# Kernel tuning notes

Hardware: AMD Instinct MI355X
Metric: run time of the kernel (lower is better)

Reference implementation:

```python
import jax, jax.numpy as jnp
import numpy as np

B, T, H, NH = 4, 2048, 2048, 16
HD = H // NH
SCALE = HD ** -0.5

def setup_inputs() -> dict:
    key = jax.random.key(0)
    ks = jax.random.split(key, 9)
    s = H ** -0.5
    return {
        "x": jax.random.normal(ks[0], (B, T, H), jnp.float32),
        "q_w": jax.random.normal(ks[1], (H, H), jnp.float32) * s,
        "q_b": jnp.zeros((H,), jnp.float32),
        "k_w": jax.random.normal(ks[2], (H, H), jnp.float32) * s,
        "k_b": jnp.zeros((H,), jnp.float32),
        "v_w": jax.random.normal(ks[3], (H, H), jnp.float32) * s,
        "v_b": jnp.zeros((H,), jnp.float32),
        "o_w": jax.random.normal(ks[4], (H, H), jnp.float32) * s,
        "o_b": jnp.zeros((H,), jnp.float32),
    }

def reference(x, q_w, q_b, k_w, k_b, v_w, v_b, o_w, o_b):
    Bd, Td, Hd = x.shape
    # projections (torch Linear: y = x @ W^T + b)
    q = (x @ q_w.T + q_b).reshape(Bd, Td, NH, HD).transpose(0, 2, 1, 3)  # [B,nh,T,hd]
    k = (x @ k_w.T + k_b).reshape(Bd, Td, NH, HD).transpose(0, 2, 1, 3)
    v = (x @ v_w.T + v_b).reshape(Bd, Td, NH, HD).transpose(0, 2, 1, 3)
    scores = jnp.einsum('bhqd,bhkd->bhqk', q, k) * SCALE  # [B,nh,T,T]
    causal = jnp.tril(jnp.ones((Td, Td), dtype=bool))
    scores = jnp.where(causal, scores, -jnp.inf)
    probs = jax.nn.softmax(scores, axis=-1)
    ctx = jnp.einsum('bhqk,bhkd->bhqd', probs, v)  # [B,nh,T,hd]
    ctx = ctx.transpose(0, 2, 1, 3).reshape(Bd, Td, Hd)
    return ctx @ o_w.T + o_b
```

## Files before the change

### kernel.cpp

```cpp
#include <hip/hip_runtime.h>
#include <stdint.h>

#define B_SZ 4
#define T_SEQ 2048
#define H_DIM 2048
#define NH_ 16
#define HD_ 128
#define MTOK (B_SZ * T_SEQ)

typedef __attribute__((ext_vector_type(8))) short bf16x8;
typedef __attribute__((ext_vector_type(4))) float f32x4;
typedef __attribute__((ext_vector_type(4))) unsigned short u16x4;

__device__ __forceinline__ unsigned short f2b(float f) {
  union { float f; uint32_t u; } x; x.f = f;
  uint32_t r = x.u + 0x7FFFu + ((x.u >> 16) & 1u);
  return (unsigned short)(r >> 16);
}

__device__ __forceinline__ void gload16(const void* g, void* l) {
  __builtin_amdgcn_global_load_lds((const __attribute__((address_space(1))) void*)g,
                                   (__attribute__((address_space(3))) void*)l, 16, 0, 0);
}

__global__ void cvt_bf16_k(const float* __restrict__ in, unsigned short* __restrict__ out, int n4) {
  for (int i = blockIdx.x * blockDim.x + threadIdx.x; i < n4; i += gridDim.x * blockDim.x) {
    float4 v = ((const float4*)in)[i];
    u16x4 o;
    o[0] = f2b(v.x); o[1] = f2b(v.y); o[2] = f2b(v.z); o[3] = f2b(v.w);
    ((u16x4*)out)[i] = o;
  }
}

__global__ void cvt4_bf16_k(const float* __restrict__ s0, const float* __restrict__ s1,
                            const float* __restrict__ s2, const float* __restrict__ s3,
                            unsigned short* __restrict__ d0, unsigned short* __restrict__ d1,
                            unsigned short* __restrict__ d2, unsigned short* __restrict__ d3) {
  const int n4each = (H_DIM * H_DIM) / 4;
  for (int i = blockIdx.x * blockDim.x + threadIdx.x; i < 4 * n4each; i += gridDim.x * blockDim.x) {
    int sel = i >> 20, j = i & (n4each - 1);
    const float* src = sel == 0 ? s0 : sel == 1 ? s1 : sel == 2 ? s2 : s3;
    unsigned short* dst = sel == 0 ? d0 : sel == 1 ? d1 : sel == 2 ? d2 : d3;
    float4 v = ((const float4*)src)[j];
    u16x4 o;
    o[0] = f2b(v.x); o[1] = f2b(v.y); o[2] = f2b(v.z); o[3] = f2b(v.w);
    ((u16x4*)dst)[j] = o;
  }
}

template <int MODE>
__global__ __launch_bounds__(512, 2) void gemm256_k(const unsigned short* __restrict__ A,
                                                    const unsigned short* __restrict__ W,
                                                    const float* __restrict__ bias,
                                                    void* __restrict__ outp,
                                                    float oscale) {
  constexpr int K = H_DIM;
  constexpr int NT = K / 64;
  __shared__ __align__(16) unsigned short Al[2][256 * 64];
  __shared__ __align__(16) unsigned short Bl[2][256 * 64];

  const int tid = threadIdx.x;
  const int w = tid >> 6, l = tid & 63;
  const int g = l >> 4, ln = l & 15;
  const int wr = w >> 2, wc = w & 3;

  const int bid = blockIdx.x + gridDim.x * blockIdx.y;
  const int fid = ((bid & 7) << 5) | (bid >> 3);
  const int col0 = (fid & 7) * 256;
  const int row0 = (fid >> 3) * 256;

  const char* Ag = (const char*)A;
  const char* Wg = (const char*)W;

  const int srow = l >> 3;
  const int sbyte = ((l & 7) * 16) ^ (srow << 4);

#define ST_A(t2, b2, c)                                                                 \
  gload16(Ag + (((size_t)(row0 + (c) * 8 + srow)) * K + (t2) * 64) * 2 + sbyte,         \
          (char*)&Al[b2][0] + (c) * 1024)
#define ST_B(t2, b2, c)                                                                 \
  gload16(Wg + (((size_t)(col0 + (c) * 8 + srow)) * K + (t2) * 64) * 2 + sbyte,         \
          (char*)&Bl[b2][0] + (c) * 1024)
#define STAGE_A0(t2, b2) do { ST_A(t2, b2, w);  ST_A(t2, b2, 16 + w); } while (0)
#define STAGE_A1(t2, b2) do { ST_A(t2, b2, 8 + w); ST_A(t2, b2, 24 + w); } while (0)
#define STAGE_B0(t2, b2) do { int c_ = (w >> 2) * 8 + (w & 3); ST_B(t2, b2, c_); ST_B(t2, b2, 16 + c_); } while (0)
#define STAGE_B1(t2, b2) do { int c_ = (w >> 2) * 8 + 4 + (w & 3); ST_B(t2, b2, c_); ST_B(t2, b2, 16 + c_); } while (0)

  f32x4 acc[8][4] = {};
  bf16x8 aF[4][2];
  bf16x8 bF[2][2][2];

#define READ_A(mh)                                                                      \
  _Pragma("unroll") for (int mf = 0; mf < 4; ++mf)                                      \
  _Pragma("unroll") for (int ks = 0; ks < 2; ++ks) {                                    \
    int row_ = wr * 128 + (mh) * 64 + mf * 16 + ln;                                     \
    aF[mf][ks] = *(const bf16x8*)((const char*)Ab + row_ * 128 +                        \
                                  ((ks * 64 + g * 16) ^ ((ln & 7) << 4)));              \
  }
#define READ_B(nh)                                                                      \
  _Pragma("unroll") for (int nf = 0; nf < 2; ++nf)                                      \
  _Pragma("unroll") for (int ks = 0; ks < 2; ++ks) {                                    \
    int row_ = wc * 64 + (nh) * 32 + nf * 16 + ln;                                      \
    bF[nh][nf][ks] = *(const bf16x8*)((const char*)Bb + row_ * 128 +                    \
                                      ((ks * 64 + g * 16) ^ ((ln & 7) << 4)));          \
  }
#define MFMA_PHASE(mh, nh)                                                              \
  do {                                                                                  \
    __builtin_amdgcn_s_setprio(1);                                                      \
    _Pragma("unroll") for (int mf = 0; mf < 4; ++mf)                                    \
    _Pragma("unroll") for (int nf = 0; nf < 2; ++nf)                                    \
    _Pragma("unroll") for (int ks = 0; ks < 2; ++ks)                                    \
      acc[(mh) * 4 + mf][(nh) * 2 + nf] = __builtin_amdgcn_mfma_f32_16x16x32_bf16(      \
          aF[mf][ks], bF[nh][nf][ks], acc[(mh) * 4 + mf][(nh) * 2 + nf], 0, 0, 0);      \
    __builtin_amdgcn_s_setprio(0);                                                      \
  } while (0)
#define BARRIER() asm volatile("s_barrier" ::: "memory")

  STAGE_A0(0, 0); STAGE_B0(0, 0); STAGE_B1(0, 0); STAGE_A1(0, 0);
  STAGE_A0(1, 1); STAGE_B0(1, 1); STAGE_B1(1, 1); STAGE_A1(1, 1);
  asm volatile("s_waitcnt vmcnt(8)" ::: "memory");
  BARRIER();

#pragma unroll 1
  for (int t = 0; t < NT; ++t) {
    const int buf = t & 1;
    const unsigned short* Ab = &Al[buf][0];
    const unsigned short* Bb = &Bl[buf][0];
    READ_A(0); READ_B(0);
    if (t >= 1 && t + 1 < NT) STAGE_A1(t + 1, (t + 1) & 1);
    BARRIER();
    MFMA_PHASE(0, 0);
    BARRIER();
    READ_B(1);
    if (t + 2 < NT) STAGE_A0(t + 2, buf);
    BARRIER();
    MFMA_PHASE(0, 1);
    BARRIER();
    READ_A(1);
    if (t + 2 < NT) STAGE_B0(t + 2, buf);
    BARRIER();
    MFMA_PHASE(1, 0);
    BARRIER();
    if (t + 2 < NT) {
      STAGE_B1(t + 2, buf);
      asm volatile("s_waitcnt vmcnt(6)" ::: "memory");
    } else {
      asm volatile("s_waitcnt vmcnt(0)" ::: "memory");
    }
    BARRIER();
    MFMA_PHASE(1, 1);
    BARRIER();
  }

#pragma unroll
  for (int mi = 0; mi < 8; ++mi) {
#pragma unroll
    for (int ni = 0; ni < 4; ++ni) {
      int n = col0 + wc * 64 + ni * 16 + ln;
      float bv = bias[n];
      if constexpr (MODE == 2) {
        float* out = (float*)outp;
#pragma unroll
        for (int r = 0; r < 4; ++r) {
          int m = row0 + wr * 128 + mi * 16 + 4 * g + r;
          out[(size_t)m * H_DIM + n] = acc[mi][ni][r] + bv;
        }
      } else if constexpr (MODE == 0) {
        unsigned short* out = (unsigned short*)outp;
        int h = n >> 7, d = n & 127;
#pragma unroll
        for (int r = 0; r < 4; ++r) {
          int m = row0 + wr * 128 + mi * 16 + 4 * g + r;
          int b = m >> 11, tt = m & 2047;
          out[(((size_t)(b * NH_ + h)) * T_SEQ + tt) * HD_ + d] = f2b((acc[mi][ni][r] + bv) * oscale);
        }
      } else if constexpr (MODE == 3) {
        unsigned short* out = (unsigned short*)outp;
        int h = n >> 7, d = n & 127;
#pragma unroll
        for (int r = 0; r < 4; ++r) {
          int m = row0 + wr * 128 + mi * 16 + 4 * g + r;
          int b = m >> 11, tt = m & 2047;
          int tl = tt & 63;
          int tp = (tt & ~63) | ((tl >> 5) * 32 + ((tl >> 2) & 1) * 16 + ((tl >> 3) & 3) * 4 + (tl & 3));
          out[(((size_t)(b * NH_ + h)) * T_SEQ + tp) * HD_ + d] = f2b(acc[mi][ni][r] + bv);
        }
      } else {
        unsigned short* out = (unsigned short*)outp;
        int h = n >> 7, d = n & 127;
        int m0 = row0 + wr * 128 + mi * 16 + 4 * g;
        int b = m0 >> 11, t0 = m0 & 2047;
        u16x4 pk;
#pragma unroll
        for (int r = 0; r < 4; ++r) pk[r] = f2b(acc[mi][ni][r] + bv);
        *(u16x4*)&out[(((size_t)(b * NH_ + h)) * HD_ + d) * T_SEQ + t0] = pk;
      }
    }
  }
#undef ST_A
#undef ST_B
#undef STAGE_A0
#undef STAGE_A1
#undef STAGE_B0
#undef STAGE_B1
#undef READ_A
#undef READ_B
#undef MFMA_PHASE
#undef BARRIER
}

__global__ __launch_bounds__(512, 2) void attn256_k(const unsigned short* __restrict__ Q,
                                                    const unsigned short* __restrict__ Kg,
                                                    const unsigned short* __restrict__ Vt,
                                                    unsigned short* __restrict__ ctx) {
  __shared__ __align__(16) unsigned short Kl[2][64 * 128];
  __shared__ __align__(16) unsigned short Vl[2][128 * 64];

  const int tid = threadIdx.x;
  const int w = tid >> 6, l = tid & 63;
  const int g = l >> 4, ln = l & 15;

  const int flat = ((blockIdx.x & 7) << 5) | (blockIdx.x >> 3);
  const int qi = flat & 3;
  const int bh = flat >> 2;

  const char* kbase = (const char*)(Kg + (size_t)bh * T_SEQ * HD_);
  const char* vbase = (const char*)(Vt + (size_t)bh * HD_ * T_SEQ);
  const int b = bh >> 4, h = bh & 15;

#define STAGE_KV(bufi, ktile) do {                                                    \
    int kv0_ = (ktile) * 64;                                                          \
    _Pragma("unroll")                                                                 \
    for (int i_ = 0; i_ < 2; ++i_) {                                                  \
      int c_ = w * 2 + i_;                                                            \
      int kvr_ = c_ * 4 + g;                                                          \
      gload16(kbase + ((size_t)(kv0_ + kvr_) * HD_) * 2 + ((ln * 16) ^ ((kvr_ & 7) << 4)), \
              (char*)&Kl[bufi][0] + c_ * 1024);                                       \
      int d_ = c_ * 8 + (l >> 3);                                                     \
      gload16(vbase + ((size_t)d_ * T_SEQ + kv0_) * 2 + (((l & 7) * 16) ^ ((d_ & 7) << 4)), \
              (char*)&Vl[bufi][0] + c_ * 1024);                                       \
    } } while (0)

#pragma unroll 1
  for (int half = 0; half < 2; ++half) {
    const int qt = half ? qi : (7 - qi);
    const int q0 = qt << 8;
    const int qw = q0 + w * 32;

    bf16x8 bq[2][4];
#pragma unroll
    for (int f = 0; f < 2; ++f)
#pragma unroll
      for (int kk = 0; kk < 4; ++kk)
        bq[f][kk] = *(const bf16x8*)(Q + ((size_t)bh * T_SEQ + qw + f * 16 + ln) * HD_ + kk * 32 + g * 8);

    f32x4 acc[2][8] = {};
    float mrun[2] = {-INFINITY, -INFINITY};
    float lrun[2] = {0.f, 0.f};

    const int nt = (qt + 1) * 4;

    STAGE_KV(0, 0);
    __syncthreads();
    int cur = 0;

#pragma unroll 1
    for (int kt = 0; kt < nt; ++kt) {
      if (kt + 1 < nt) STAGE_KV(cur ^ 1, kt + 1);
      const int kv0 = kt * 64;
      if (kv0 <= qw + 31) {
        const char* kl = (const char*)&Kl[cur][0];
        const char* vl = (const char*)&Vl[cur][0];

        f32x4 st[2][4] = {};
        __builtin_amdgcn_s_setprio(1);
#pragma unroll
        for (int kk = 0; kk < 4; ++kk) {
          bf16x8 ak[4];
#pragma unroll
          for (int mf = 0; mf < 4; ++mf)
            ak[mf] = *(const bf16x8*)(kl + (mf * 16 + ln) * 256 + ((kk * 64 + g * 16) ^ ((ln & 7) << 4)));
#pragma unroll
          for (int mf = 0; mf < 4; ++mf) {
            st[0][mf] = __builtin_amdgcn_mfma_f32_16x16x32_bf16(ak[mf], bq[0][kk], st[0][mf], 0, 0, 0);
            st[1][mf] = __builtin_amdgcn_mfma_f32_16x16x32_bf16(ak[mf], bq[1][kk], st[1][mf], 0, 0, 0);
          }
        }
        __builtin_amdgcn_s_setprio(0);

        if (kv0 + 63 > qw) {
#pragma unroll
          for (int f = 0; f < 2; ++f)
#pragma unroll
            for (int mf = 0; mf < 4; ++mf)
#pragma unroll
              for (int r = 0; r < 4; ++r)
                if (kv0 + 32 * (mf >> 1) + 8 * g + 4 * (mf & 1) + r > qw + f * 16 + ln)
                  st[f][mf][r] = -INFINITY;
        }

        bf16x8 ap[2][2];
#pragma unroll
        for (int f = 0; f < 2; ++f) {
          float pmax = -INFINITY;
#pragma unroll
          for (int mf = 0; mf < 4; ++mf)
#pragma unroll
            for (int r = 0; r < 4; ++r) pmax = fmaxf(pmax, st[f][mf][r]);
          pmax = fmaxf(pmax, __shfl_xor(pmax, 16));
          pmax = fmaxf(pmax, __shfl_xor(pmax, 32));
          float msub = mrun[f];
          if (__any(pmax > mrun[f] + 8.f)) {
            msub = fmaxf(mrun[f], pmax);
            float fac = __builtin_amdgcn_exp2f(mrun[f] - msub);
            mrun[f] = msub;
            lrun[f] *= fac;
            float fr[4];
#pragma unroll
            for (int r = 0; r < 4; ++r) fr[r] = __shfl(fac, g * 4 + r);
#pragma unroll
            for (int nf = 0; nf < 8; ++nf) {
              acc[f][nf][0] *= fr[0]; acc[f][nf][1] *= fr[1];
              acc[f][nf][2] *= fr[2]; acc[f][nf][3] *= fr[3];
            }
          }
          uint32_t Aq[4][2];
          float psum = 0.f;
#pragma unroll
          for (int mf = 0; mf < 4; ++mf) {
            float p0 = __builtin_amdgcn_exp2f(st[f][mf][0] - msub);
            float p1 = __builtin_amdgcn_exp2f(st[f][mf][1] - msub);
            float p2 = __builtin_amdgcn_exp2f(st[f][mf][2] - msub);
            float p3 = __builtin_amdgcn_exp2f(st[f][mf][3] - msub);
            psum += (p0 + p1) + (p2 + p3);
            asm("v_cvt_pk_bf16_f32 %0, %1, %2" : "=v"(Aq[mf][0]) : "v"(p0), "v"(p1));
            asm("v_cvt_pk_bf16_f32 %0, %1, %2" : "=v"(Aq[mf][1]) : "v"(p2), "v"(p3));
          }
          psum += __shfl_xor(psum, 16);
          psum += __shfl_xor(psum, 32);
          lrun[f] += psum;

#pragma unroll
          for (int ks = 0; ks < 2; ++ks) {
            union { uint32_t u[4]; bf16x8 v; } t;
            t.u[0] = Aq[2 * ks][0];     t.u[1] = Aq[2 * ks][1];
            t.u[2] = Aq[2 * ks + 1][0]; t.u[3] = Aq[2 * ks + 1][1];
            ap[f][ks] = t.v;
          }
        }

        __builtin_amdgcn_s_setprio(1);
#pragma unroll
        for (int nf = 0; nf < 8; ++nf) {
          int d = nf * 16 + ln;
#pragma unroll
          for (int ks = 0; ks < 2; ++ks) {
            bf16x8 bv = *(const bf16x8*)(vl + d * 128 + ((ks * 64 + g * 16) ^ ((ln & 7) << 4)));
            acc[0][nf] = __builtin_amdgcn_mfma_f32_16x16x32_bf16(ap[0][ks], bv, acc[0][nf], 0, 0, 0);
            acc[1][nf] = __builtin_amdgcn_mfma_f32_16x16x32_bf16(ap[1][ks], bv, acc[1][nf], 0, 0, 0);
          }
        }
        __builtin_amdgcn_s_setprio(0);
      }
      __syncthreads();
      cur ^= 1;
    }

#pragma unroll
    for (int f = 0; f < 2; ++f) {
      float inv[4];
#pragma unroll
      for (int r = 0; r < 4; ++r) inv[r] = 1.f / __shfl(lrun[f], g * 4 + r);
#pragma unroll
      for (int nf = 0; nf < 8; ++nf) {
#pragma unroll
        for (int r = 0; r < 4; ++r) {
          int qrow = qw + f * 16 + g * 4 + r;
          ctx[((size_t)(b * T_SEQ + qrow)) * H_DIM + h * HD_ + nf * 16 + ln] =
              f2b(acc[f][nf][r] * inv[r]);
        }
      }
    }
  }
#undef STAGE_KV
}

extern "C" void kernel_launch(void* const* d_in, const int* in_sizes, int n_in,
                              void* d_out, int out_size, void* d_ws, size_t ws_size,
                              hipStream_t stream) {
  (void)in_sizes; (void)n_in; (void)out_size; (void)ws_size;
  const float* x  = (const float*)d_in[0];
  const float* qw = (const float*)d_in[1];
  const float* qb = (const float*)d_in[2];
  const float* kw = (const float*)d_in[3];
  const float* kb = (const float*)d_in[4];
  const float* vw = (const float*)d_in[5];
  const float* vb = (const float*)d_in[6];
  const float* ow = (const float*)d_in[7];
  const float* ob = (const float*)d_in[8];

  char* ws = (char*)d_ws;
  unsigned short* xb  = (unsigned short*)(ws);
  unsigned short* qwb = (unsigned short*)(ws + 33554432);
  unsigned short* kwb = (unsigned short*)(ws + 41943040);
  unsigned short* vwb = (unsigned short*)(ws + 50331648);
  unsigned short* owb = (unsigned short*)(ws + 58720256);
  unsigned short* Qb  = (unsigned short*)(ws + 67108864);
  unsigned short* Kb  = (unsigned short*)(ws + 100663296);
  unsigned short* Vtb = (unsigned short*)(ws + 134217728);
  unsigned short* ctxb = xb;

  const float cscale = 0.08838834764831845f * 1.4426950408889634f;

  dim3 blk(256);
  cvt_bf16_k<<<2048, blk, 0, stream>>>(x, xb, (MTOK * H_DIM) / 4);
  cvt4_bf16_k<<<2048, blk, 0, stream>>>(qw, kw, vw, ow, qwb, kwb, vwb, owb);

  dim3 ggrid(H_DIM / 256, MTOK / 256);
  dim3 gblk(512);
  gemm256_k<0><<<ggrid, gblk, 0, stream>>>(xb, qwb, qb, Qb, cscale);
  gemm256_k<3><<<ggrid, gblk, 0, stream>>>(xb, kwb, kb, Kb, 1.0f);
  gemm256_k<1><<<ggrid, gblk, 0, stream>>>(xb, vwb, vb, Vtb, 1.0f);

  attn256_k<<<dim3(256), dim3(512), 0, stream>>>(Qb, Kb, Vtb, ctxb);

  gemm256_k<2><<<ggrid, gblk, 0, stream>>>(ctxb, owb, ob, (float*)d_out, 1.0f);
}
```

Before: 388.5 us.

## Restructure GEMM main loop to overlap LDS reads with MFMA phases

Reworks the projection GEMM's K-loop schedule so that LDS fragment reads for the next phase are issued right after or alongside the current MFMA phase, halves the number of barriers per iteration, and peels the last two iterations into an explicit epilogue. The next tile's first A/B fragments are prefetched at the end of each iteration. The goal is to hide LDS latency and cut barrier stalls. The cost is a more fragile hand-tuned wait/barrier ordering, with a risk of races, since STAGE_A0 into the current buffer is issued while READ_A(1) on that buffer is still pending.

```diff
diff --git a/kernel.cpp b/kernel.cpp
--- a/kernel.cpp
+++ b/kernel.cpp
@@ -90,66 +90,94 @@
   bf16x8 aF[4][2];
   bf16x8 bF[2][2][2];
 
-#define READ_A(mh)                                                                      \
-  _Pragma("unroll") for (int mf = 0; mf < 4; ++mf)                                      \
-  _Pragma("unroll") for (int ks = 0; ks < 2; ++ks) {                                    \
-    int row_ = wr * 128 + (mh) * 64 + mf * 16 + ln;                                     \
-    aF[mf][ks] = *(const bf16x8*)((const char*)Ab + row_ * 128 +                        \
-                                  ((ks * 64 + g * 16) ^ ((ln & 7) << 4)));              \
-  }
-#define READ_B(nh)                                                                      \
-  _Pragma("unroll") for (int nf = 0; nf < 2; ++nf)                                      \
-  _Pragma("unroll") for (int ks = 0; ks < 2; ++ks) {                                    \
-    int row_ = wc * 64 + (nh) * 32 + nf * 16 + ln;                                      \
-    bF[nh][nf][ks] = *(const bf16x8*)((const char*)Bb + row_ * 128 +                    \
-                                      ((ks * 64 + g * 16) ^ ((ln & 7) << 4)));          \
-  }
-#define MFMA_PHASE(mh, nh)                                                              \
+#define READ_A(mh, SRC)                                                                 \
+  _Pragma("unroll") for (int mf_ = 0; mf_ < 4; ++mf_)                                   \
+  _Pragma("unroll") for (int ks_ = 0; ks_ < 2; ++ks_) {                                 \
+    int row_ = wr * 128 + (mh) * 64 + mf_ * 16 + ln;                                    \
+    aF[mf_][ks_] = *(const bf16x8*)((SRC) + row_ * 128 +                                \
+                                    ((ks_ * 64 + g * 16) ^ ((ln & 7) << 4)));           \
+  }
+#define READ_Bn(nh, SRC)                                                                \
+  _Pragma("unroll") for (int nf_ = 0; nf_ < 2; ++nf_)                                   \
+  _Pragma("unroll") for (int ks_ = 0; ks_ < 2; ++ks_) {                                 \
+    int row_ = wc * 64 + (nh) * 32 + nf_ * 16 + ln;                                     \
+    bF[nh][nf_][ks_] = *(const bf16x8*)((SRC) + row_ * 128 +                            \
+                                        ((ks_ * 64 + g * 16) ^ ((ln & 7) << 4)));       \
+  }
+#define MFMA_PH(mh, nh)                                                                 \
   do {                                                                                  \
     __builtin_amdgcn_s_setprio(1);                                                      \
-    _Pragma("unroll") for (int mf = 0; mf < 4; ++mf)                                    \
-    _Pragma("unroll") for (int nf = 0; nf < 2; ++nf)                                    \
-    _Pragma("unroll") for (int ks = 0; ks < 2; ++ks)                                    \
-      acc[(mh) * 4 + mf][(nh) * 2 + nf] = __builtin_amdgcn_mfma_f32_16x16x32_bf16(      \
-          aF[mf][ks], bF[nh][nf][ks], acc[(mh) * 4 + mf][(nh) * 2 + nf], 0, 0, 0);      \
+    _Pragma("unroll") for (int mf_ = 0; mf_ < 4; ++mf_)                                 \
+    _Pragma("unroll") for (int nf_ = 0; nf_ < 2; ++nf_)                                 \
+    _Pragma("unroll") for (int ks_ = 0; ks_ < 2; ++ks_)                                 \
+      acc[(mh) * 4 + mf_][(nh) * 2 + nf_] = __builtin_amdgcn_mfma_f32_16x16x32_bf16(    \
+          aF[mf_][ks_], bF[nh][nf_][ks_], acc[(mh) * 4 + mf_][(nh) * 2 + nf_],          \
+          0, 0, 0);                                                                     \
     __builtin_amdgcn_s_setprio(0);                                                      \
   } while (0)
+#define WAITV(n) asm volatile("s_waitcnt vmcnt(" #n ")" ::: "memory")
+#define WAITL()  asm volatile("s_waitcnt lgkmcnt(0)" ::: "memory")
 #define BARRIER() asm volatile("s_barrier" ::: "memory")
 
-  STAGE_A0(0, 0); STAGE_B0(0, 0); STAGE_B1(0, 0); STAGE_A1(0, 0);
-  STAGE_A0(1, 1); STAGE_B0(1, 1); STAGE_B1(1, 1); STAGE_A1(1, 1);
-  asm volatile("s_waitcnt vmcnt(8)" ::: "memory");
+  STAGE_A0(0, 0); STAGE_B0(0, 0); STAGE_A1(0, 0); STAGE_B1(0, 0);
+  WAITV(0);
   BARRIER();
+  READ_A(0, (const char*)&Al[0][0]);
+  READ_Bn(0, (const char*)&Bl[0][0]);
+  STAGE_A0(1, 1); STAGE_B0(1, 1); STAGE_A1(1, 1); STAGE_B1(1, 1);
+  WAITL();
 
 #pragma unroll 1
-  for (int t = 0; t < NT; ++t) {
+  for (int t = 0; t < NT - 2; ++t) {
     const int buf = t & 1;
-    const unsigned short* Ab = &Al[buf][0];
-    const unsigned short* Bb = &Bl[buf][0];
-    READ_A(0); READ_B(0);
-    if (t >= 1 && t + 1 < NT) STAGE_A1(t + 1, (t + 1) & 1);
-    BARRIER();
-    MFMA_PHASE(0, 0);
-    BARRIER();
-    READ_B(1);
-    if (t + 2 < NT) STAGE_A0(t + 2, buf);
-    BARRIER();
-    MFMA_PHASE(0, 1);
-    BARRIER();
-    READ_A(1);
-    if (t + 2 < NT) STAGE_B0(t + 2, buf);
-    BARRIER();
-    MFMA_PHASE(1, 0);
-    BARRIER();
-    if (t + 2 < NT) {
-      STAGE_B1(t + 2, buf);
-      asm volatile("s_waitcnt vmcnt(6)" ::: "memory");
-    } else {
-      asm volatile("s_waitcnt vmcnt(0)" ::: "memory");
-    }
-    BARRIER();
-    MFMA_PHASE(1, 1);
-    BARRIER();
+    const char* cA = (const char*)&Al[buf][0];
+    const char* cB = (const char*)&Bl[buf][0];
+    const char* nA = (const char*)&Al[buf ^ 1][0];
+    const char* nB = (const char*)&Bl[buf ^ 1][0];
+    WAITV(6); BARRIER();
+    READ_Bn(1, cB);
+    STAGE_A0(t + 2, buf);
+    MFMA_PH(0, 0);
+    WAITV(6); BARRIER();
+    MFMA_PH(0, 1);
+    READ_A(1, cA);
+    STAGE_B0(t + 2, buf);
+    WAITL();
+    WAITV(6); BARRIER();
+    STAGE_A1(t + 2, buf);
+    MFMA_PH(1, 0);
+    WAITV(6); BARRIER();
+    MFMA_PH(1, 1);
+    READ_A(0, nA);
+    READ_Bn(0, nB);
+    STAGE_B1(t + 2, buf);
+    WAITL();
+  }
+
+  {
+    const char* cA = (const char*)&Al[0][0];
+    const char* cB = (const char*)&Bl[0][0];
+    const char* nA = (const char*)&Al[1][0];
+    const char* nB = (const char*)&Bl[1][0];
+    READ_Bn(1, cB);
+    MFMA_PH(0, 0);
+    MFMA_PH(0, 1);
+    READ_A(1, cA);
+    MFMA_PH(1, 0);
+    WAITV(0); BARRIER();
+    MFMA_PH(1, 1);
+    READ_A(0, nA);
+    READ_Bn(0, nB);
+  }
+  {
+    const char* nA = (const char*)&Al[1][0];
+    const char* nB = (const char*)&Bl[1][0];
+    READ_Bn(1, nB);
+    MFMA_PH(0, 0);
+    MFMA_PH(0, 1);
+    READ_A(1, nA);
+    MFMA_PH(1, 0);
+    MFMA_PH(1, 1);
   }
 
 #pragma unroll
@@ -204,8 +232,10 @@
 #undef STAGE_B0
 #undef STAGE_B1
 #undef READ_A
-#undef READ_B
-#undef MFMA_PHASE
+#undef READ_Bn
+#undef MFMA_PH
+#undef WAITV
+#undef WAITL
 #undef BARRIER
 }
 
```

Result: no change. 394.0 us (+1.4%).
